# Kernel tuning notes

Hardware: AMD Instinct MI355X
Metric: run time of the kernel (lower is better)

Reference implementation:

```python
import jax, jax.numpy as jnp
import numpy as np

EMBEDDING_DIM = 128
NEG = -1000.0


def setup_inputs() -> dict:
    key = jax.random.key(0)
    ks = jax.random.split(key, 7)
    B, S_src, S_tgt, D = 2, 4096, 512, EMBEDDING_DIM
    return {
        "input_embeddings": jax.random.normal(ks[0], (B, S_src, D), dtype=jnp.float32),
        "token_attention_masks_source": jax.random.randint(ks[1], (B, S_src), 0, 2, dtype=jnp.int32),
        "token_attention_masks_target": jax.random.randint(ks[2], (B, S_tgt), 0, 2, dtype=jnp.int32),
        "encoder_output_embedding": jax.random.normal(ks[3], (B, S_tgt, D), dtype=jnp.float32),
        "w_query": jax.random.uniform(ks[4], (D, D), dtype=jnp.float32),
        "w_key": jax.random.uniform(ks[5], (D, D), dtype=jnp.float32),
        "w_value": jax.random.uniform(ks[6], (D, D), dtype=jnp.float32),
    }


def reference(input_embeddings, token_attention_masks_source,
              token_attention_masks_target, encoder_output_embedding,
              w_query, w_key, w_value):
    # Encoder self-attention branch (attention_type='encoder'), num_heads=1.
    D = w_query.shape[0]
    q = jnp.einsum('bsd,de->bse', input_embeddings, w_query)   # [B,S,D]
    k = jnp.einsum('bsd,de->bse', input_embeddings, w_key)     # [B,S,D]
    v = jnp.einsum('bsd,de->bse', input_embeddings, w_value)   # [B,S,D]
    scores = jnp.einsum('bsd,btd->bst', q, k) / jnp.sqrt(jnp.float32(D))
    # Original adds mask along the QUERY axis: mask[B,S] -> unsqueeze(-1).
    add_mask = jnp.where(token_attention_masks_source == 0, NEG, 0.0).astype(scores.dtype)
    scores = scores + add_mask[:, :, None]
    probs = jax.nn.softmax(scores, axis=2)                      # softmax over keys
    out = jnp.einsum('bst,btd->bsd', probs, v)                  # [B,S,D]
    return out
```

## Files before the change

### kernel.cpp

```cpp
#include <hip/hip_runtime.h>
#include <hip/hip_bf16.h>

#define S_SRC 4096
#define DIM 128
#define BATCH 2
#define NSP 8
#define NQB 32
#define NQG 512
#define NITER 16

typedef unsigned short u16;
typedef unsigned int u32;
typedef __bf16 bf16x8 __attribute__((ext_vector_type(8)));
typedef float f32x4 __attribute__((ext_vector_type(4)));
typedef u32 u32x4 __attribute__((ext_vector_type(4)));
typedef u16 u16x4 __attribute__((ext_vector_type(4)));

__device__ __forceinline__ __bf16 bf_hi(float x) { return (__bf16)x; }
__device__ __forceinline__ __bf16 bf_lo(float x, __bf16 h) { return (__bf16)(x - (float)h); }
__device__ __forceinline__ u16 bfu(__bf16 h) { return __builtin_bit_cast(u16, h); }
__device__ __forceinline__ u16 f2bu(float x) { return __builtin_bit_cast(u16, (__bf16)x); }
__device__ __forceinline__ float bu2f(u16 u) { return (float)__builtin_bit_cast(__bf16, u); }
__device__ __forceinline__ u32 pk2(float lo, float hi) {
  return (u32)f2bu(lo) | ((u32)f2bu(hi) << 16);
}
__device__ __forceinline__ void g2l16(const u16* src, u16* ldst) {
  __builtin_amdgcn_global_load_lds((const __attribute__((address_space(1))) void*)src,
                                   (__attribute__((address_space(3))) void*)ldst, 16, 0, 0);
}
#define MFMA __builtin_amdgcn_mfma_f32_16x16x32_bf16

__global__ __launch_bounds__(256) void k_wsplit(const float* __restrict__ wq,
                                                const float* __restrict__ wk,
                                                const float* __restrict__ wv,
                                                u16* __restrict__ wt) {
  int idx = blockIdx.x * 256 + threadIdx.x;
  int mat = idx >> 14;
  int r = idx & 16383;
  int d = r >> 7, e = r & 127;
  const float* w = (mat == 0) ? wq : ((mat == 1) ? wk : wv);
  float x = w[r];
  if (mat == 0) x *= 0.08838834764831845f;
  __bf16 h = bf_hi(x);
  __bf16 l = bf_lo(x, h);
  wt[((mat * 2 + 0) * 128 + e) * 128 + d] = bfu(h);
  wt[((mat * 2 + 1) * 128 + e) * 128 + d] = bfu(l);
}

__global__ __launch_bounds__(256) void k_proj(const float* __restrict__ X,
                                              const u16* __restrict__ wt,
                                              u16* __restrict__ Qh, u16* __restrict__ Ql,
                                              u16* __restrict__ Kh, u16* __restrict__ Kl,
                                              u16* __restrict__ VT) {
  const int mat = blockIdx.x >> 8;
  const int t = blockIdx.x & 255;
  const int b = t >> 7;
  const int tile = t & 127;
  const int tid = threadIdx.x;
  const int w = tid >> 6, lane = tid & 63, g = lane >> 4, l16 = lane & 15;

  bf16x8 a_h[2][4], a_l[2][4];
#pragma unroll
  for (int mf = 0; mf < 2; ++mf) {
    int row = tile * 32 + mf * 16 + l16;
    const float* xr = X + ((size_t)b * S_SRC + row) * DIM;
#pragma unroll
    for (int kf = 0; kf < 4; ++kf) {
      int d0 = kf * 32 + g * 8;
      f32x4 x0 = *(const f32x4*)(xr + d0);
      f32x4 x1 = *(const f32x4*)(xr + d0 + 4);
#pragma unroll
      for (int j = 0; j < 4; ++j) {
        __bf16 h0 = bf_hi(x0[j]);
        __bf16 h1 = bf_hi(x1[j]);
        a_h[mf][kf][j] = h0;
        a_l[mf][kf][j] = bf_lo(x0[j], h0);
        a_h[mf][kf][4 + j] = h1;
        a_l[mf][kf][4 + j] = bf_lo(x1[j], h1);
      }
    }
  }

  const u16* wth = wt + (mat * 2 + 0) * 16384;
  const u16* wtl = wt + (mat * 2 + 1) * 16384;
#pragma unroll
  for (int nf = 0; nf < 2; ++nf) {
    int col = w * 32 + nf * 16 + l16;
    f32x4 acc[2];
    acc[0] = (f32x4){0.f, 0.f, 0.f, 0.f};
    acc[1] = (f32x4){0.f, 0.f, 0.f, 0.f};
#pragma unroll
    for (int kf = 0; kf < 4; ++kf) {
      int d0 = kf * 32 + g * 8;
      bf16x8 bh = *(const bf16x8*)(const void*)(wth + col * 128 + d0);
      bf16x8 bl = *(const bf16x8*)(const void*)(wtl + col * 128 + d0);
#pragma unroll
      for (int mf = 0; mf < 2; ++mf) {
        acc[mf] = MFMA(a_h[mf][kf], bh, acc[mf], 0, 0, 0);
        acc[mf] = MFMA(a_h[mf][kf], bl, acc[mf], 0, 0, 0);
        acc[mf] = MFMA(a_l[mf][kf], bh, acc[mf], 0, 0, 0);
      }
    }
#pragma unroll
    for (int mf = 0; mf < 2; ++mf)
#pragma unroll
      for (int r = 0; r < 4; ++r) {
        int row = tile * 32 + mf * 16 + g * 4 + r;
        float v = acc[mf][r];
        if (mat == 2) {
          VT[((size_t)b * DIM + col) * S_SRC + row] = f2bu(v);
        } else {
          __bf16 h = bf_hi(v);
          __bf16 l = bf_lo(v, h);
          size_t o = ((size_t)b * S_SRC + row) * DIM + col;
          if (mat == 0) { Qh[o] = bfu(h); Ql[o] = bfu(l); }
          else          { Kh[o] = bfu(h); Kl[o] = bfu(l); }
        }
      }
  }
}

__device__ __forceinline__ void qk_tile(const u16* kb, int g, int l16,
                                        const bf16x8 qh0[4], const bf16x8 ql0[4],
                                        const bf16x8 qh1[4], const bf16x8 ql1[4],
                                        f32x4& s00, f32x4& s01, f32x4& s10, f32x4& s11) {
  s00 = s01 = s10 = s11 = (f32x4){0.f, 0.f, 0.f, 0.f};
  __builtin_amdgcn_s_setprio(1);
#pragma unroll
  for (int kf = 0; kf < 4; ++kf) {
    int cs = ((kf * 4 + g) ^ l16) << 3;
    bf16x8 kh0 = *(const bf16x8*)(const void*)(kb + l16 * 128 + cs);
    bf16x8 kl0 = *(const bf16x8*)(const void*)(kb + 4096 + l16 * 128 + cs);
    s00 = MFMA(kh0, qh0[kf], s00, 0, 0, 0);
    s00 = MFMA(kh0, ql0[kf], s00, 0, 0, 0);
    s00 = MFMA(kl0, qh0[kf], s00, 0, 0, 0);
    s10 = MFMA(kh0, qh1[kf], s10, 0, 0, 0);
    s10 = MFMA(kh0, ql1[kf], s10, 0, 0, 0);
    s10 = MFMA(kl0, qh1[kf], s10, 0, 0, 0);
    bf16x8 kh1 = *(const bf16x8*)(const void*)(kb + (16 + l16) * 128 + cs);
    bf16x8 kl1 = *(const bf16x8*)(const void*)(kb + 4096 + (16 + l16) * 128 + cs);
    s01 = MFMA(kh1, qh0[kf], s01, 0, 0, 0);
    s01 = MFMA(kh1, ql0[kf], s01, 0, 0, 0);
    s01 = MFMA(kl1, qh0[kf], s01, 0, 0, 0);
    s11 = MFMA(kh1, qh1[kf], s11, 0, 0, 0);
    s11 = MFMA(kh1, ql1[kf], s11, 0, 0, 0);
    s11 = MFMA(kl1, qh1[kf], s11, 0, 0, 0);
  }
  __builtin_amdgcn_s_setprio(0);
}

__device__ __forceinline__ void sm_pack(f32x4 sA, f32x4 sB, float& mr, float& lr,
                                        f32x4 acc[8], int g, bf16x8& pa) {
  float mx = fmaxf(fmaxf(fmaxf(sA[0], sA[1]), fmaxf(sA[2], sA[3])),
                   fmaxf(fmaxf(sB[0], sB[1]), fmaxf(sB[2], sB[3])));
  mx = fmaxf(mx, __shfl_xor(mx, 16, 64));
  mx = fmaxf(mx, __shfl_xor(mx, 32, 64));
  if (!__all(mx - mr <= 8.0f)) {
    float mn = fmaxf(mr, mx);
    float f = __expf(mr - mn);
    lr *= f;
    mr = mn;
    float fr0 = __shfl(f, g * 4 + 0, 64);
    float fr1 = __shfl(f, g * 4 + 1, 64);
    float fr2 = __shfl(f, g * 4 + 2, 64);
    float fr3 = __shfl(f, g * 4 + 3, 64);
#pragma unroll
    for (int nf = 0; nf < 8; ++nf) {
      acc[nf][0] *= fr0; acc[nf][1] *= fr1; acc[nf][2] *= fr2; acc[nf][3] *= fr3;
    }
  }
  float e0 = __expf(sA[0] - mr), e1 = __expf(sA[1] - mr);
  float e2 = __expf(sA[2] - mr), e3 = __expf(sA[3] - mr);
  float e4 = __expf(sB[0] - mr), e5 = __expf(sB[1] - mr);
  float e6 = __expf(sB[2] - mr), e7 = __expf(sB[3] - mr);
  float sm = ((e0 + e1) + (e2 + e3)) + ((e4 + e5) + (e6 + e7));
  sm += __shfl_xor(sm, 16, 64);
  sm += __shfl_xor(sm, 32, 64);
  lr += sm;
  u32 w0 = pk2(e0, e1), w1 = pk2(e2, e3), w2 = pk2(e4, e5), w3 = pk2(e6, e7);
  u32 x0 = __shfl_xor(w0, 16, 64), x1 = __shfl_xor(w1, 16, 64);
  u32 x2 = __shfl_xor(w2, 16, 64), x3 = __shfl_xor(w3, 16, 64);
  bool odd = (g & 1);
  u32x4 pw;
  pw.x = odd ? x2 : w0;
  pw.y = odd ? x3 : w1;
  pw.z = odd ? w2 : x0;
  pw.w = odd ? w3 : x1;
  pa = __builtin_bit_cast(bf16x8, pw);
}

__device__ __forceinline__ void pv_tile(const u16* vb, int mg, int l16,
                                        bf16x8 pa0, bf16x8 pa1,
                                        f32x4 acc0[8], f32x4 acc1[8]) {
  __builtin_amdgcn_s_setprio(1);
#pragma unroll
  for (int nf = 0; nf < 8; ++nf) {
    int d = nf * 16 + l16;
    bf16x8 vf = *(const bf16x8*)(const void*)(vb + d * 32 + ((mg ^ ((d >> 1) & 3)) << 3));
    acc0[nf] = MFMA(pa0, vf, acc0[nf], 0, 0, 0);
    acc1[nf] = MFMA(pa1, vf, acc1[nf], 0, 0, 0);
  }
  __builtin_amdgcn_s_setprio(0);
}

__global__ __launch_bounds__(512, 2) void k_attn(const u16* __restrict__ Qh, const u16* __restrict__ Ql,
                                                 const u16* __restrict__ Kh, const u16* __restrict__ Kl,
                                                 const u16* __restrict__ VT,
                                                 float* __restrict__ Pm, float* __restrict__ Pl,
                                                 u16* __restrict__ PO) {
  const int bid = blockIdx.x;
  const int sp = bid & 7;
  const int qb = bid >> 3;
  const int b = qb >> 4;
  const int tid = threadIdx.x;
  const int w = tid >> 6, lane = tid & 63, g = lane >> 4, l16 = lane & 15;

  __shared__ alignas(16) u16 kbuf[2][8192];
  __shared__ alignas(16) u16 vbuf[3][4096];

  const int gr0 = qb * 256 + w * 32;
  bf16x8 qh0[4], ql0[4], qh1[4], ql1[4];
  {
    const u16* p0h = Qh + ((size_t)gr0 + l16) * DIM;
    const u16* p0l = Ql + ((size_t)gr0 + l16) * DIM;
    const u16* p1h = Qh + ((size_t)gr0 + 16 + l16) * DIM;
    const u16* p1l = Ql + ((size_t)gr0 + 16 + l16) * DIM;
#pragma unroll
    for (int kf = 0; kf < 4; ++kf) {
      int d0 = kf * 32 + g * 8;
      qh0[kf] = *(const bf16x8*)(const void*)(p0h + d0);
      ql0[kf] = *(const bf16x8*)(const void*)(p0l + d0);
      qh1[kf] = *(const bf16x8*)(const void*)(p1h + d0);
      ql1[kf] = *(const bf16x8*)(const void*)(p1l + d0);
    }
  }

  f32x4 acc0[8], acc1[8];
#pragma unroll
  for (int nf = 0; nf < 8; ++nf) {
    acc0[nf] = (f32x4){0.f, 0.f, 0.f, 0.f};
    acc1[nf] = (f32x4){0.f, 0.f, 0.f, 0.f};
  }
  float m0 = -1e30f, m1 = -1e30f, l0 = 0.f, l1 = 0.f;

  const int key_base = sp * (S_SRC / NSP);
  const u16* KhB = Kh + (size_t)b * S_SRC * DIM;
  const u16* KlB = Kl + (size_t)b * S_SRC * DIM;
  const u16* VTB = VT + (size_t)b * DIM * S_SRC;

  const int kkey = tid >> 4, kcp = tid & 15;
  const int kcs = (kcp ^ (kkey & 15)) << 3;
  const int vd = tid >> 2, vcp = tid & 3;
  const int vcs = (vcp ^ ((vd >> 1) & 3)) << 3;
  const int wbase = w * 512;
  const int mg = ((g & 1) << 1) | (g >> 1);

#define STAGE(KB, VB, KEY0)                                                       \
  {                                                                               \
    g2l16(KhB + ((size_t)((KEY0) + kkey)) * DIM + kcs, &kbuf[KB][wbase]);         \
    g2l16(KlB + ((size_t)((KEY0) + kkey)) * DIM + kcs, &kbuf[KB][4096 + wbase]);  \
    g2l16(VTB + (size_t)vd * S_SRC + (KEY0) + vcs,     &vbuf[VB][wbase]);         \
  }
#define WAITBAR { asm volatile("s_waitcnt vmcnt(0)" ::: "memory"); __builtin_amdgcn_s_barrier(); }

  f32x4 a00, a01, a10, a11;
  f32x4 b00, b01, b10, b11;
  bf16x8 pa0, pa1;

  STAGE(0, 0, key_base)
  STAGE(1, 1, key_base + 32)
  asm volatile("s_waitcnt vmcnt(3)" ::: "memory");
  __builtin_amdgcn_s_barrier();
  qk_tile(kbuf[0], g, l16, qh0, ql0, qh1, ql1, a00, a01, a10, a11);
  WAITBAR

  int va = 0;
  for (int ii = 0; ii < NITER - 2; ii += 2) {
    const int v1 = (va + 1) % 3, v2 = (va + 2) % 3;
    STAGE(ii & 1, v2, key_base + (ii + 2) * 32)
    qk_tile(kbuf[(ii & 1) ^ 1], g, l16, qh0, ql0, qh1, ql1, b00, b01, b10, b11);
    sm_pack(a00, a01, m0, l0, acc0, g, pa0);
    sm_pack(a10, a11, m1, l1, acc1, g, pa1);
    pv_tile(vbuf[va], mg, l16, pa0, pa1, acc0, acc1);
    WAITBAR
    STAGE((ii & 1) ^ 1, va, key_base + (ii + 3) * 32)
    qk_tile(kbuf[ii & 1], g, l16, qh0, ql0, qh1, ql1, a00, a01, a10, a11);
    sm_pack(b00, b01, m0, l0, acc0, g, pa0);
    sm_pack(b10, b11, m1, l1, acc1, g, pa1);
    pv_tile(vbuf[v1], mg, l16, pa0, pa1, acc0, acc1);
    WAITBAR
    va = v2;
  }

  {
    const int v1 = (va + 1) % 3;
    qk_tile(kbuf[1], g, l16, qh0, ql0, qh1, ql1, b00, b01, b10, b11);
    sm_pack(a00, a01, m0, l0, acc0, g, pa0);
    sm_pack(a10, a11, m1, l1, acc1, g, pa1);
    pv_tile(vbuf[va], mg, l16, pa0, pa1, acc0, acc1);
    sm_pack(b00, b01, m0, l0, acc0, g, pa0);
    sm_pack(b10, b11, m1, l1, acc1, g, pa1);
    pv_tile(vbuf[v1], mg, l16, pa0, pa1, acc0, acc1);
  }

  const int pidx0 = sp * NQG + (gr0 >> 4);
  {
    u16* po = PO + (size_t)pidx0 * 16 * DIM;
#pragma unroll
    for (int nf = 0; nf < 8; ++nf)
#pragma unroll
      for (int r = 0; r < 4; ++r)
        po[(g * 4 + r) * DIM + nf * 16 + l16] = f2bu(acc0[nf][r]);
    u16* po1 = PO + (size_t)(pidx0 + 1) * 16 * DIM;
#pragma unroll
    for (int nf = 0; nf < 8; ++nf)
#pragma unroll
      for (int r = 0; r < 4; ++r)
        po1[(g * 4 + r) * DIM + nf * 16 + l16] = f2bu(acc1[nf][r]);
  }
  if (g == 0) { Pm[pidx0 * 16 + l16] = m0; Pl[pidx0 * 16 + l16] = l0; }
  if (g == 1) { Pm[(pidx0 + 1) * 16 + l16] = m1; Pl[(pidx0 + 1) * 16 + l16] = l1; }
#undef STAGE
#undef WAITBAR
}

__global__ __launch_bounds__(64) void k_comb(const float* __restrict__ Pm,
                                             const float* __restrict__ Pl,
                                             const u16* __restrict__ PO,
                                             float* __restrict__ out) {
  const int qg = blockIdx.x;
  const int tid = threadIdx.x;

  __shared__ float sc[NSP][16];
  if (tid < 16) {
    float m = -1e30f;
#pragma unroll
    for (int s = 0; s < NSP; ++s) m = fmaxf(m, Pm[(s * NQG + qg) * 16 + tid]);
    float den = 0.f;
#pragma unroll
    for (int s = 0; s < NSP; ++s) {
      float e = __expf(Pm[(s * NQG + qg) * 16 + tid] - m);
      sc[s][tid] = e;
      den += Pl[(s * NQG + qg) * 16 + tid] * e;
    }
    float inv = 1.0f / den;
#pragma unroll
    for (int s = 0; s < NSP; ++s) sc[s][tid] *= inv;
  }
  __syncthreads();

  float* op = out + (size_t)qg * 16 * DIM;
  for (int i = tid; i < 16 * DIM / 4; i += 64) {
    int row = (i * 4) >> 7;
    f32x4 a = (f32x4){0.f, 0.f, 0.f, 0.f};
#pragma unroll
    for (int s = 0; s < NSP; ++s) {
      u16x4 p = *(const u16x4*)(const void*)(PO + (size_t)(s * NQG + qg) * 16 * DIM + i * 4);
      float wgt = sc[s][row];
      a[0] += bu2f(p.x) * wgt;
      a[1] += bu2f(p.y) * wgt;
      a[2] += bu2f(p.z) * wgt;
      a[3] += bu2f(p.w) * wgt;
    }
    *(f32x4*)(op + i * 4) = a;
  }
}

extern "C" void kernel_launch(void* const* d_in, const int* in_sizes, int n_in,
                              void* d_out, int out_size, void* d_ws, size_t ws_size,
                              hipStream_t stream) {
  const float* X  = (const float*)d_in[0];
  const float* wq = (const float*)d_in[4];
  const float* wk = (const float*)d_in[5];
  const float* wv = (const float*)d_in[6];
  float* out = (float*)d_out;

  u16* WT = (u16*)d_ws;
  u16* Qh = WT + 3 * 2 * 128 * 128;
  u16* Ql = Qh + (size_t)BATCH * S_SRC * DIM;
  u16* Kh = Ql + (size_t)BATCH * S_SRC * DIM;
  u16* Kl = Kh + (size_t)BATCH * S_SRC * DIM;
  u16* VT = Kl + (size_t)BATCH * S_SRC * DIM;
  float* Pm = (float*)(VT + (size_t)BATCH * S_SRC * DIM);
  float* Pl = Pm + (size_t)NSP * NQG * 16;
  u16* PO = (u16*)(Pl + (size_t)NSP * NQG * 16);

  hipLaunchKernelGGL(k_wsplit, dim3(192), dim3(256), 0, stream, wq, wk, wv, WT);
  hipLaunchKernelGGL(k_proj, dim3(3 * 256), dim3(256), 0, stream,
                     X, WT, Qh, Ql, Kh, Kl, VT);
  hipLaunchKernelGGL(k_attn, dim3(NQB * NSP), dim3(512), 0, stream,
                     Qh, Ql, Kh, Kl, VT, Pm, Pl, PO);
  hipLaunchKernelGGL(k_comb, dim3(NQG), dim3(64), 0, stream, Pm, Pl, PO, out);
}
```

Before: 75.20 us.

## Restructure attention main loop into 4-buffer ring with two-tile prefetch depth

Replaces the two-way unrolled K/V pipeline (2 K buffers, 3 V buffers, QK of the next tile interleaved with softmax and PV of the current one) with a uniform 4-slot ring. Each iteration issues the load two tiles ahead, waits only until that newest stage is still outstanding (vmcnt(6)), barriers, then runs QK, softmax and PV for the current tile in sequence. The aim is to keep more global-to-LDS traffic in flight and simplify the schedule. In exchange, LDS use per block rises to 96 KB, and the explicit overlap of the next tile's QK MFMAs with the current softmax is given up.

```diff
diff --git a/kernel.cpp b/kernel.cpp
--- a/kernel.cpp
+++ b/kernel.cpp
@@ -215,8 +215,8 @@
   const int tid = threadIdx.x;
   const int w = tid >> 6, lane = tid & 63, g = lane >> 4, l16 = lane & 15;
 
-  __shared__ alignas(16) u16 kbuf[2][8192];
-  __shared__ alignas(16) u16 vbuf[3][4096];
+  __shared__ alignas(16) u16 kbuf[4][8192];
+  __shared__ alignas(16) u16 vbuf[4][4096];
 
   const int gr0 = qb * 256 + w * 32;
   bf16x8 qh0[4], ql0[4], qh1[4], ql1[4];
@@ -255,53 +255,37 @@
   const int wbase = w * 512;
   const int mg = ((g & 1) << 1) | (g >> 1);
 
-#define STAGE(KB, VB, KEY0)                                                       \
-  {                                                                               \
-    g2l16(KhB + ((size_t)((KEY0) + kkey)) * DIM + kcs, &kbuf[KB][wbase]);         \
-    g2l16(KlB + ((size_t)((KEY0) + kkey)) * DIM + kcs, &kbuf[KB][4096 + wbase]);  \
-    g2l16(VTB + (size_t)vd * S_SRC + (KEY0) + vcs,     &vbuf[VB][wbase]);         \
-  }
-#define WAITBAR { asm volatile("s_waitcnt vmcnt(0)" ::: "memory"); __builtin_amdgcn_s_barrier(); }
-
-  f32x4 a00, a01, a10, a11;
-  f32x4 b00, b01, b10, b11;
-  bf16x8 pa0, pa1;
-
-  STAGE(0, 0, key_base)
-  STAGE(1, 1, key_base + 32)
+#define STAGE(BUF, KEY0)                                                        \
+  {                                                                             \
+    g2l16(KhB + ((size_t)((KEY0) + kkey)) * DIM + kcs, &kbuf[BUF][wbase]);      \
+    g2l16(KlB + ((size_t)((KEY0) + kkey)) * DIM + kcs, &kbuf[BUF][4096 + wbase]); \
+    g2l16(VTB + (size_t)vd * S_SRC + (KEY0) + vcs,     &vbuf[BUF][wbase]);      \
+  }
+#define BODY(I)                                                                  \
+  {                                                                              \
+    f32x4 s00, s01, s10, s11;                                                    \
+    qk_tile(kbuf[(I) & 3], g, l16, qh0, ql0, qh1, ql1, s00, s01, s10, s11);      \
+    bf16x8 pa0, pa1;                                                             \
+    sm_pack(s00, s01, m0, l0, acc0, g, pa0);                                     \
+    sm_pack(s10, s11, m1, l1, acc1, g, pa1);                                     \
+    pv_tile(vbuf[(I) & 3], mg, l16, pa0, pa1, acc0, acc1);                       \
+  }
+
+  STAGE(0, key_base)
+  STAGE(1, key_base + 32)
+
+  for (int i = 0; i < NITER - 2; ++i) {
+    STAGE((i + 2) & 3, key_base + (i + 2) * 32)
+    asm volatile("s_waitcnt vmcnt(6)" ::: "memory");
+    __builtin_amdgcn_s_barrier();
+    BODY(i)
+  }
   asm volatile("s_waitcnt vmcnt(3)" ::: "memory");
   __builtin_amdgcn_s_barrier();
-  qk_tile(kbuf[0], g, l16, qh0, ql0, qh1, ql1, a00, a01, a10, a11);
-  WAITBAR
-
-  int va = 0;
-  for (int ii = 0; ii < NITER - 2; ii += 2) {
-    const int v1 = (va + 1) % 3, v2 = (va + 2) % 3;
-    STAGE(ii & 1, v2, key_base + (ii + 2) * 32)
-    qk_tile(kbuf[(ii & 1) ^ 1], g, l16, qh0, ql0, qh1, ql1, b00, b01, b10, b11);
-    sm_pack(a00, a01, m0, l0, acc0, g, pa0);
-    sm_pack(a10, a11, m1, l1, acc1, g, pa1);
-    pv_tile(vbuf[va], mg, l16, pa0, pa1, acc0, acc1);
-    WAITBAR
-    STAGE((ii & 1) ^ 1, va, key_base + (ii + 3) * 32)
-    qk_tile(kbuf[ii & 1], g, l16, qh0, ql0, qh1, ql1, a00, a01, a10, a11);
-    sm_pack(b00, b01, m0, l0, acc0, g, pa0);
-    sm_pack(b10, b11, m1, l1, acc1, g, pa1);
-    pv_tile(vbuf[v1], mg, l16, pa0, pa1, acc0, acc1);
-    WAITBAR
-    va = v2;
-  }
-
-  {
-    const int v1 = (va + 1) % 3;
-    qk_tile(kbuf[1], g, l16, qh0, ql0, qh1, ql1, b00, b01, b10, b11);
-    sm_pack(a00, a01, m0, l0, acc0, g, pa0);
-    sm_pack(a10, a11, m1, l1, acc1, g, pa1);
-    pv_tile(vbuf[va], mg, l16, pa0, pa1, acc0, acc1);
-    sm_pack(b00, b01, m0, l0, acc0, g, pa0);
-    sm_pack(b10, b11, m1, l1, acc1, g, pa1);
-    pv_tile(vbuf[v1], mg, l16, pa0, pa1, acc0, acc1);
-  }
+  BODY(NITER - 2)
+  asm volatile("s_waitcnt vmcnt(0)" ::: "memory");
+  __builtin_amdgcn_s_barrier();
+  BODY(NITER - 1)
 
   const int pidx0 = sp * NQG + (gr0 >> 4);
   {
@@ -321,7 +305,7 @@
   if (g == 0) { Pm[pidx0 * 16 + l16] = m0; Pl[pidx0 * 16 + l16] = l0; }
   if (g == 1) { Pm[(pidx0 + 1) * 16 + l16] = m1; Pl[(pidx0 + 1) * 16 + l16] = l1; }
 #undef STAGE
-#undef WAITBAR
+#undef BODY
 }
 
 __global__ __launch_bounds__(64) void k_comb(const float* __restrict__ Pm,
```

New measurement: 74.60 us. No clear change (-0.8%).
